# Kernel tuning notes

Hardware: AMD Instinct MI355X
Metric: run time of the kernel (lower is better)

## Reference

```python
import jax, jax.numpy as jnp
import numpy as np

NUM_CAPSULE = 32
DIM_CAPSULE = 32
ROUTINGS = 3
T_EPSILON = 1e-7


def setup_inputs() -> dict:
    key = jax.random.key(0)
    k1, k2 = jax.random.split(key)
    x = jax.random.normal(k1, (64, 1024, 256), dtype=jnp.float32)
    # xavier_normal_ on [1, 256, 32*32]: std = sqrt(2/(fan_in+fan_out)) = sqrt(2/(256+1024))
    std = np.sqrt(2.0 / (256 + NUM_CAPSULE * DIM_CAPSULE)).astype(np.float32)
    W = jax.random.normal(k2, (1, 256, NUM_CAPSULE * DIM_CAPSULE), dtype=jnp.float32) * std
    return {"x": x, "W": W}


def _squash(v, eps):
    # x / sqrt(sum(x^2) + eps)  (note: not the classic squash; faithful to source)
    s = jnp.sum(v * v, axis=-1, keepdims=True)
    return v / jnp.sqrt(s + eps)


def reference(x, W):
    B, N_in, _ = x.shape
    # u_hat: [B, num_capsule, input_num_capsule, dim_capsule]
    u_hat = jnp.matmul(x, W).reshape(B, N_in, NUM_CAPSULE, DIM_CAPSULE)
    u_hat = jnp.transpose(u_hat, (0, 2, 1, 3))
    b = jnp.zeros(u_hat.shape[:3], dtype=u_hat.dtype)  # [B, num, n_in]
    outputs = None
    for i in range(ROUTINGS):
        # original: softmax over the num_capsule axis (dim=2 after permute(0,2,1))
        c = jax.nn.softmax(b, axis=1)  # [B, num, n_in]
        outputs = _squash(jnp.einsum('bij,bijk->bik', c, u_hat), T_EPSILON)  # [B, num, dim]
        if i < ROUTINGS - 1:
            b = jnp.einsum('bik,bijk->bij', outputs, u_hat)
    return outputs
```

## Files before the change

kernel.cpp:

```cpp
#include <hip/hip_runtime.h>
#include <cstdint>
#include <cstddef>

#define BATCH 64
#define NIN   1024
#define CIN   256
#define NC    32
#define NJC   16
#define JCH   64
#define T_EPS 1e-7f
#define CT_S  72

typedef __attribute__((ext_vector_type(8))) short short8;
typedef __attribute__((ext_vector_type(4))) float floatx4;

__device__ __forceinline__ unsigned short bf16rne(float f) {
  unsigned int u = __float_as_uint(f);
  u += 0x7FFFu + ((u >> 16) & 1u);
  return (unsigned short)(u >> 16);
}
__device__ __forceinline__ float bf2f(unsigned short h) {
  return __uint_as_float(((unsigned int)h) << 16);
}
__device__ __forceinline__ int xsw(int j, int c) {
  return j * 256 + ((((c >> 3) ^ (j & 7) ^ ((j >> 3) & 7)) << 3) | (c & 7));
}

__global__ __launch_bounds__(256) void k_convert(const float* __restrict__ x,
                                                 const float* __restrict__ W,
                                                 unsigned short* __restrict__ xb,
                                                 unsigned short* __restrict__ Wi,
                                                 float* __restrict__ y0p) {
  const int jc = blockIdx.x, b = blockIdx.y, t = threadIdx.x;
  const int jj = t >> 6, c4 = t & 63;
  __shared__ float4 red[4][64];
  const float4* xg = (const float4*)(x + ((size_t)(b * NIN + jc * JCH)) * CIN);
  ushort4* xo = (ushort4*)(xb + ((size_t)(b * NIN + jc * JCH)) * CIN);
  float4 acc = make_float4(0.f, 0.f, 0.f, 0.f);
  #pragma unroll
  for (int jr = 0; jr < 16; ++jr) {
    int j = jr * 4 + jj;
    float4 v = xg[j * 64 + c4];
    acc.x += v.x; acc.y += v.y; acc.z += v.z; acc.w += v.w;
    ushort4 h;
    h.x = bf16rne(v.x); h.y = bf16rne(v.y);
    h.z = bf16rne(v.z); h.w = bf16rne(v.w);
    xo[j * 64 + c4] = h;
  }
  red[jj][c4] = acc;
  if (b == 0) {
    #pragma unroll
    for (int i2 = 0; i2 < 2; ++i2) {
      int i = jc * 2 + i2;
      const float4* wsrc = (const float4*)(W + (size_t)t * 1024 + i * 32);
      unsigned short* wdst = Wi + ((size_t)i * CIN + t) * NC;
      #pragma unroll
      for (int k4 = 0; k4 < 8; ++k4) {
        float4 v = wsrc[k4];
        ushort4 h;
        h.x = bf16rne(v.x); h.y = bf16rne(v.y);
        h.z = bf16rne(v.z); h.w = bf16rne(v.w);
        *(ushort4*)&wdst[k4 * 4] = h;
      }
    }
  }
  __syncthreads();
  if (t < 64) {
    float4 s = red[0][t];
    #pragma unroll
    for (int p = 1; p < 4; ++p) {
      s.x += red[p][t].x; s.y += red[p][t].y;
      s.z += red[p][t].z; s.w += red[p][t].w;
    }
    *(float4*)&y0p[(b * NJC + jc) * CIN + t * 4] = s;
  }
}

template <int MODE>
__global__ __launch_bounds__(256) void k_post(const void* __restrict__ yin,
                                              const unsigned short* __restrict__ Wi,
                                              unsigned short* __restrict__ wtout,
                                              float* __restrict__ outg) {
  const int i = blockIdx.x, b = blockIdx.y, t = threadIdx.x;
  __shared__ float ys[CIN];
  __shared__ float sred[8][32];
  __shared__ float os[NC];
  float a = 0.f;
  if (MODE == 0) {
    const float* y0p = (const float*)yin;
    #pragma unroll
    for (int p = 0; p < NJC; ++p) a += y0p[(b * NJC + p) * CIN + t];
    a *= (1.f / 32.f);
  } else {
    const unsigned short* yp = (const unsigned short*)yin;
    #pragma unroll
    for (int p = 0; p < NJC; ++p)
      a += bf2f(yp[(((size_t)(b * NJC + p)) * NC + i) * CIN + t]);
  }
  ys[t] = a;
  __syncthreads();
  const unsigned short* Wis = Wi + (size_t)i * CIN * NC;
  {
    const int k = t & 31, g = t >> 5;
    float ps = 0.f;
    #pragma unroll
    for (int cc = 0; cc < 32; ++cc) {
      int c = g * 32 + ((cc + g * 4) & 31);
      ps += ys[c] * bf2f(Wis[c * NC + k]);
    }
    sred[g][k] = ps;
  }
  __syncthreads();
  const int k = t & 31;
  float s = 0.f;
  #pragma unroll
  for (int g = 0; g < 8; ++g) s += sred[g][k];
  float s2 = s * s;
  #pragma unroll
  for (int m = 1; m < 32; m <<= 1) s2 += __shfl_xor(s2, m);
  float o = s * rsqrtf(s2 + T_EPS);
  if (MODE == 2) {
    if (t < 32) outg[((size_t)b * NC + i) * 32 + t] = o;
  } else {
    if (t < 32) os[t] = o;
    __syncthreads();
    float acc = 0.f;
    const short8* wrow = (const short8*)(Wis + (size_t)t * NC);
    #pragma unroll
    for (int k8 = 0; k8 < 4; ++k8) {
      short8 wv = wrow[k8];
      #pragma unroll
      for (int e = 0; e < 8; ++e)
        acc += os[k8 * 8 + e] * bf2f((unsigned short)wv[e]);
    }
    wtout[((size_t)b * NC + i) * CIN + t] = bf16rne(acc);
  }
}

__global__ __launch_bounds__(256, 4) void k_fused(const unsigned short* __restrict__ xb,
                                                  const unsigned short* __restrict__ wt,
                                                  unsigned short* __restrict__ ypart) {
  const int jc = blockIdx.x, b = blockIdx.y, t = threadIdx.x;
  const int w = t >> 6, l16 = t & 15, q = (t >> 4) & 3;
  __shared__ unsigned short xs[64 * 256];
  __shared__ unsigned short cT[NC * CT_S];
  {
    const short8* xg =
        (const short8*)(xb + ((size_t)(b * NIN) + (size_t)jc * JCH) * CIN);
    #pragma unroll
    for (int it = 0; it < 8; ++it) {
      int f = it * 256 + t;
      int j = f >> 5, ch = f & 31;
      *(short8*)&xs[xsw(j, ch * 8)] = xg[f];
    }
  }
  const int jloc = w * 16 + l16;
  const unsigned short* wrow = wt + (size_t)b * NC * CIN;
  floatx4 accA0 = {0.f, 0.f, 0.f, 0.f}, accA1 = {0.f, 0.f, 0.f, 0.f};
  __syncthreads();
  #pragma unroll
  for (int ks = 0; ks < 8; ++ks) {
    short8 bx = *(const short8*)&xs[xsw(jloc, ks * 32 + q * 8)];
    short8 a0 = *(const short8*)(wrow + (size_t)l16 * CIN + ks * 32 + q * 8);
    short8 a1 = *(const short8*)(wrow + (size_t)(16 + l16) * CIN + ks * 32 + q * 8);
    accA0 = __builtin_amdgcn_mfma_f32_16x16x32_bf16(a0, bx, accA0, 0, 0, 0);
    accA1 = __builtin_amdgcn_mfma_f32_16x16x32_bf16(a1, bx, accA1, 0, 0, 0);
  }
  {
    float m = accA0[0];
    #pragma unroll
    for (int r = 1; r < 4; ++r) m = fmaxf(m, accA0[r]);
    #pragma unroll
    for (int r = 0; r < 4; ++r) m = fmaxf(m, accA1[r]);
    m = fmaxf(m, __shfl_xor(m, 16));
    m = fmaxf(m, __shfl_xor(m, 32));
    float e0[4], e1[4], s = 0.f;
    #pragma unroll
    for (int r = 0; r < 4; ++r) {
      e0[r] = __expf(accA0[r] - m);
      e1[r] = __expf(accA1[r] - m);
      s += e0[r] + e1[r];
    }
    s += __shfl_xor(s, 16);
    s += __shfl_xor(s, 32);
    float rs = 1.f / s;
    #pragma unroll
    for (int r = 0; r < 4; ++r) {
      cT[(q * 4 + r) * CT_S + jloc]      = bf16rne(e0[r] * rs);
      cT[(16 + q * 4 + r) * CT_S + jloc] = bf16rne(e1[r] * rs);
    }
  }
  __syncthreads();
  const int cw = w * 64;
  floatx4 accB[2][4];
  #pragma unroll
  for (int h = 0; h < 2; ++h)
    #pragma unroll
    for (int ct = 0; ct < 4; ++ct) accB[h][ct] = (floatx4){0.f, 0.f, 0.f, 0.f};
  #pragma unroll
  for (int ks = 0; ks < 2; ++ks) {
    short8 ca0 = *(const short8*)&cT[l16 * CT_S + ks * 32 + q * 8];
    short8 ca1 = *(const short8*)&cT[(16 + l16) * CT_S + ks * 32 + q * 8];
    #pragma unroll
    for (int ct = 0; ct < 4; ++ct) {
      const int c = cw + ct * 16 + l16;
      short8 xf;
      #pragma unroll
      for (int e = 0; e < 8; ++e)
        xf[e] = (short)xs[xsw(ks * 32 + q * 8 + e, c)];
      accB[0][ct] = __builtin_amdgcn_mfma_f32_16x16x32_bf16(ca0, xf, accB[0][ct], 0, 0, 0);
      accB[1][ct] = __builtin_amdgcn_mfma_f32_16x16x32_bf16(ca1, xf, accB[1][ct], 0, 0, 0);
    }
  }
  unsigned short* yo = ypart + ((size_t)(b * NJC + jc)) * NC * CIN;
  #pragma unroll
  for (int h = 0; h < 2; ++h)
    #pragma unroll
    for (int ct = 0; ct < 4; ++ct)
      #pragma unroll
      for (int r = 0; r < 4; ++r) {
        int i = h * 16 + q * 4 + r;
        int c = cw + ct * 16 + l16;
        yo[i * CIN + c] = bf16rne(accB[h][ct][r]);
      }
}

extern "C" void kernel_launch(void* const* d_in, const int* in_sizes, int n_in,
                              void* d_out, int out_size, void* d_ws, size_t ws_size,
                              hipStream_t stream) {
  (void)in_sizes; (void)n_in; (void)out_size; (void)ws_size;
  const float* x = (const float*)d_in[0];
  const float* W = (const float*)d_in[1];
  float* out = (float*)d_out;
  char* ws = (char*)d_ws;
  unsigned short* xbuf  = (unsigned short*)ws;
  unsigned short* wtb   = (unsigned short*)(ws + (32ull << 20));
  unsigned short* ypart = (unsigned short*)(ws + (33ull << 20));
  float*          y0p   = (float*)(ws + (49ull << 20));
  unsigned short* Wi    = (unsigned short*)(ws + (50ull << 20));

  dim3 gfuse(NJC, BATCH);
  dim3 gpost(NC, BATCH);
  k_convert<<<gfuse, 256, 0, stream>>>(x, W, xbuf, Wi, y0p);
  k_post<0><<<gpost, 256, 0, stream>>>(y0p, Wi, wtb, nullptr);
  k_fused<<<gfuse, 256, 0, stream>>>(xbuf, wtb, ypart);
  k_post<1><<<gpost, 256, 0, stream>>>(ypart, Wi, wtb, nullptr);
  k_fused<<<gfuse, 256, 0, stream>>>(xbuf, wtb, ypart);
  k_post<2><<<gpost, 256, 0, stream>>>(ypart, Wi, nullptr, out);
}
```

Before: 154.5 us.

## Process two 64-row chunks per fused block, halving partial outputs

```diff
diff --git a/kernel.cpp b/kernel.cpp
--- a/kernel.cpp
+++ b/kernel.cpp
@@ -6,8 +6,8 @@
 #define NIN   1024
 #define CIN   256
 #define NC    32
-#define NJC   16
-#define JCH   64
+#define NP0   16
+#define NPF   8
 #define T_EPS 1e-7f
 #define CT_S  72
 
@@ -34,8 +34,8 @@
   const int jc = blockIdx.x, b = blockIdx.y, t = threadIdx.x;
   const int jj = t >> 6, c4 = t & 63;
   __shared__ float4 red[4][64];
-  const float4* xg = (const float4*)(x + ((size_t)(b * NIN + jc * JCH)) * CIN);
-  ushort4* xo = (ushort4*)(xb + ((size_t)(b * NIN + jc * JCH)) * CIN);
+  const float4* xg = (const float4*)(x + ((size_t)(b * NIN + jc * 64)) * CIN);
+  ushort4* xo = (ushort4*)(xb + ((size_t)(b * NIN + jc * 64)) * CIN);
   float4 acc = make_float4(0.f, 0.f, 0.f, 0.f);
   #pragma unroll
   for (int jr = 0; jr < 16; ++jr) {
@@ -72,7 +72,7 @@
       s.x += red[p][t].x; s.y += red[p][t].y;
       s.z += red[p][t].z; s.w += red[p][t].w;
     }
-    *(float4*)&y0p[(b * NJC + jc) * CIN + t * 4] = s;
+    *(float4*)&y0p[(b * NP0 + jc) * CIN + t * 4] = s;
   }
 }
 
@@ -89,13 +89,13 @@
   if (MODE == 0) {
     const float* y0p = (const float*)yin;
     #pragma unroll
-    for (int p = 0; p < NJC; ++p) a += y0p[(b * NJC + p) * CIN + t];
+    for (int p = 0; p < NP0; ++p) a += y0p[(b * NP0 + p) * CIN + t];
     a *= (1.f / 32.f);
   } else {
     const unsigned short* yp = (const unsigned short*)yin;
     #pragma unroll
-    for (int p = 0; p < NJC; ++p)
-      a += bf2f(yp[(((size_t)(b * NJC + p)) * NC + i) * CIN + t]);
+    for (int p = 0; p < NPF; ++p)
+      a += bf2f(yp[(((size_t)(b * NPF + p)) * NC + i) * CIN + t]);
   }
   ys[t] = a;
   __syncthreads();
@@ -137,82 +137,92 @@
   }
 }
 
-__global__ __launch_bounds__(256, 4) void k_fused(const unsigned short* __restrict__ xb,
+__global__ __launch_bounds__(256, 3) void k_fused(const unsigned short* __restrict__ xb,
                                                   const unsigned short* __restrict__ wt,
                                                   unsigned short* __restrict__ ypart) {
   const int jc = blockIdx.x, b = blockIdx.y, t = threadIdx.x;
   const int w = t >> 6, l16 = t & 15, q = (t >> 4) & 3;
   __shared__ unsigned short xs[64 * 256];
   __shared__ unsigned short cT[NC * CT_S];
-  {
-    const short8* xg =
-        (const short8*)(xb + ((size_t)(b * NIN) + (size_t)jc * JCH) * CIN);
-    #pragma unroll
-    for (int it = 0; it < 8; ++it) {
-      int f = it * 256 + t;
-      int j = f >> 5, ch = f & 31;
-      *(short8*)&xs[xsw(j, ch * 8)] = xg[f];
-    }
-  }
   const int jloc = w * 16 + l16;
+  const int cw = w * 64;
   const unsigned short* wrow = wt + (size_t)b * NC * CIN;
-  floatx4 accA0 = {0.f, 0.f, 0.f, 0.f}, accA1 = {0.f, 0.f, 0.f, 0.f};
-  __syncthreads();
-  #pragma unroll
-  for (int ks = 0; ks < 8; ++ks) {
-    short8 bx = *(const short8*)&xs[xsw(jloc, ks * 32 + q * 8)];
-    short8 a0 = *(const short8*)(wrow + (size_t)l16 * CIN + ks * 32 + q * 8);
-    short8 a1 = *(const short8*)(wrow + (size_t)(16 + l16) * CIN + ks * 32 + q * 8);
-    accA0 = __builtin_amdgcn_mfma_f32_16x16x32_bf16(a0, bx, accA0, 0, 0, 0);
-    accA1 = __builtin_amdgcn_mfma_f32_16x16x32_bf16(a1, bx, accA1, 0, 0, 0);
-  }
-  {
-    float m = accA0[0];
-    #pragma unroll
-    for (int r = 1; r < 4; ++r) m = fmaxf(m, accA0[r]);
-    #pragma unroll
-    for (int r = 0; r < 4; ++r) m = fmaxf(m, accA1[r]);
-    m = fmaxf(m, __shfl_xor(m, 16));
-    m = fmaxf(m, __shfl_xor(m, 32));
-    float e0[4], e1[4], s = 0.f;
-    #pragma unroll
-    for (int r = 0; r < 4; ++r) {
-      e0[r] = __expf(accA0[r] - m);
-      e1[r] = __expf(accA1[r] - m);
-      s += e0[r] + e1[r];
-    }
-    s += __shfl_xor(s, 16);
-    s += __shfl_xor(s, 32);
-    float rs = 1.f / s;
-    #pragma unroll
-    for (int r = 0; r < 4; ++r) {
-      cT[(q * 4 + r) * CT_S + jloc]      = bf16rne(e0[r] * rs);
-      cT[(16 + q * 4 + r) * CT_S + jloc] = bf16rne(e1[r] * rs);
-    }
-  }
-  __syncthreads();
-  const int cw = w * 64;
   floatx4 accB[2][4];
   #pragma unroll
   for (int h = 0; h < 2; ++h)
     #pragma unroll
     for (int ct = 0; ct < 4; ++ct) accB[h][ct] = (floatx4){0.f, 0.f, 0.f, 0.f};
-  #pragma unroll
-  for (int ks = 0; ks < 2; ++ks) {
-    short8 ca0 = *(const short8*)&cT[l16 * CT_S + ks * 32 + q * 8];
-    short8 ca1 = *(const short8*)&cT[(16 + l16) * CT_S + ks * 32 + q * 8];
-    #pragma unroll
-    for (int ct = 0; ct < 4; ++ct) {
-      const int c = cw + ct * 16 + l16;
-      short8 xf;
-      #pragma unroll
-      for (int e = 0; e < 8; ++e)
-        xf[e] = (short)xs[xsw(ks * 32 + q * 8 + e, c)];
-      accB[0][ct] = __builtin_amdgcn_mfma_f32_16x16x32_bf16(ca0, xf, accB[0][ct], 0, 0, 0);
-      accB[1][ct] = __builtin_amdgcn_mfma_f32_16x16x32_bf16(ca1, xf, accB[1][ct], 0, 0, 0);
-    }
-  }
-  unsigned short* yo = ypart + ((size_t)(b * NJC + jc)) * NC * CIN;
+
+  #pragma unroll
+  for (int sub = 0; sub < 2; ++sub) {
+    __syncthreads();
+    {
+      const short8* xg = (const short8*)(
+          xb + ((size_t)(b * NIN) + (size_t)jc * 128 + sub * 64) * CIN);
+      #pragma unroll
+      for (int it = 0; it < 8; ++it) {
+        int f = it * 256 + t;
+        int j = f >> 5, ch = f & 31;
+        *(short8*)&xs[xsw(j, ch * 8)] = xg[f];
+      }
+    }
+    __syncthreads();
+    floatx4 accA0 = {0.f, 0.f, 0.f, 0.f}, accA1 = {0.f, 0.f, 0.f, 0.f};
+    #pragma unroll
+    for (int ks = 0; ks < 8; ++ks) {
+      short8 bx = *(const short8*)&xs[xsw(jloc, ks * 32 + q * 8)];
+      short8 a0 = *(const short8*)(wrow + (size_t)l16 * CIN + ks * 32 + q * 8);
+      short8 a1 = *(const short8*)(wrow + (size_t)(16 + l16) * CIN + ks * 32 + q * 8);
+      accA0 = __builtin_amdgcn_mfma_f32_16x16x32_bf16(a0, bx, accA0, 0, 0, 0);
+      accA1 = __builtin_amdgcn_mfma_f32_16x16x32_bf16(a1, bx, accA1, 0, 0, 0);
+    }
+    short8 xf[2][4];
+    #pragma unroll
+    for (int ks = 0; ks < 2; ++ks)
+      #pragma unroll
+      for (int ct = 0; ct < 4; ++ct) {
+        const int c = cw + ct * 16 + l16;
+        #pragma unroll
+        for (int e = 0; e < 8; ++e)
+          xf[ks][ct][e] = (short)xs[xsw(ks * 32 + q * 8 + e, c)];
+      }
+    {
+      float m = accA0[0];
+      #pragma unroll
+      for (int r = 1; r < 4; ++r) m = fmaxf(m, accA0[r]);
+      #pragma unroll
+      for (int r = 0; r < 4; ++r) m = fmaxf(m, accA1[r]);
+      m = fmaxf(m, __shfl_xor(m, 16));
+      m = fmaxf(m, __shfl_xor(m, 32));
+      float e0[4], e1[4], s = 0.f;
+      #pragma unroll
+      for (int r = 0; r < 4; ++r) {
+        e0[r] = __expf(accA0[r] - m);
+        e1[r] = __expf(accA1[r] - m);
+        s += e0[r] + e1[r];
+      }
+      s += __shfl_xor(s, 16);
+      s += __shfl_xor(s, 32);
+      float rs = 1.f / s;
+      #pragma unroll
+      for (int r = 0; r < 4; ++r) {
+        cT[(q * 4 + r) * CT_S + jloc]      = bf16rne(e0[r] * rs);
+        cT[(16 + q * 4 + r) * CT_S + jloc] = bf16rne(e1[r] * rs);
+      }
+    }
+    __syncthreads();
+    #pragma unroll
+    for (int ks = 0; ks < 2; ++ks) {
+      short8 ca0 = *(const short8*)&cT[l16 * CT_S + ks * 32 + q * 8];
+      short8 ca1 = *(const short8*)&cT[(16 + l16) * CT_S + ks * 32 + q * 8];
+      #pragma unroll
+      for (int ct = 0; ct < 4; ++ct) {
+        accB[0][ct] = __builtin_amdgcn_mfma_f32_16x16x32_bf16(ca0, xf[ks][ct], accB[0][ct], 0, 0, 0);
+        accB[1][ct] = __builtin_amdgcn_mfma_f32_16x16x32_bf16(ca1, xf[ks][ct], accB[1][ct], 0, 0, 0);
+      }
+    }
+  }
+  unsigned short* yo = ypart + ((size_t)(b * NPF + jc)) * NC * CIN;
   #pragma unroll
   for (int h = 0; h < 2; ++h)
     #pragma unroll
@@ -236,12 +246,13 @@
   unsigned short* xbuf  = (unsigned short*)ws;
   unsigned short* wtb   = (unsigned short*)(ws + (32ull << 20));
   unsigned short* ypart = (unsigned short*)(ws + (33ull << 20));
-  float*          y0p   = (float*)(ws + (49ull << 20));
-  unsigned short* Wi    = (unsigned short*)(ws + (50ull << 20));
-
-  dim3 gfuse(NJC, BATCH);
+  float*          y0p   = (float*)(ws + (43ull << 20));
+  unsigned short* Wi    = (unsigned short*)(ws + (44ull << 20));
+
+  dim3 gconv(NP0, BATCH);
+  dim3 gfuse(NPF, BATCH);
   dim3 gpost(NC, BATCH);
-  k_convert<<<gfuse, 256, 0, stream>>>(x, W, xbuf, Wi, y0p);
+  k_convert<<<gconv, 256, 0, stream>>>(x, W, xbuf, Wi, y0p);
   k_post<0><<<gpost, 256, 0, stream>>>(y0p, Wi, wtb, nullptr);
   k_fused<<<gfuse, 256, 0, stream>>>(xbuf, wtb, ypart);
   k_post<1><<<gpost, 256, 0, stream>>>(ypart, Wi, wtb, nullptr);
```

New measurement: 157.4 us. Within noise of the previous version (+1.9%).
